# Optimization experiments

Hardware: AMD Instinct MI355X
Metric: run time of the kernel (lower is better)

The kernel has to match this reference:

```python
import jax, jax.numpy as jnp
import numpy as np

D_MODEL = 1024
NHEAD = 16
NUM_KV = 4
D_K = D_MODEL // NHEAD          # 64
GROUP = NHEAD // NUM_KV          # 4 query heads per kv head
ROPE_BASE = 10000.0


def _rope(x, seq_len):
    """Apply rotary embedding. x: [B, h, S, d_k], positions 0..seq_len-1."""
    half = D_K // 2
    inv_freq = 1.0 / (ROPE_BASE ** (jnp.arange(0, D_K, 2, dtype=jnp.float32) / D_K))
    t = jnp.arange(seq_len, dtype=jnp.float32)
    freqs = jnp.outer(t, inv_freq)                      # [S, d_k/2]
    emb = jnp.concatenate([freqs, freqs], axis=-1)      # [S, d_k]
    cos, sin = jnp.cos(emb), jnp.sin(emb)               # broadcast over B, h
    x1, x2 = x[..., :half], x[..., half:]
    rot = jnp.concatenate([-x2, x1], axis=-1)
    return x * cos + rot * sin


def setup_inputs() -> dict:
    key = jax.random.key(0)
    ks = jax.random.split(key, 12)
    B, S = 2, 2048
    s_in = 1.0 / np.sqrt(D_MODEL)
    inp = {
        "query": jax.random.normal(ks[0], (B, S, D_MODEL), jnp.float32),
        "key":   jax.random.normal(ks[1], (B, S, D_MODEL), jnp.float32),
        "value": jax.random.normal(ks[2], (B, S, D_MODEL), jnp.float32),
        "Wq": jax.random.normal(ks[3], (D_MODEL, D_MODEL), jnp.float32) * s_in,
        "bq": jnp.zeros((D_MODEL,), jnp.float32),
        "Wk": jax.random.normal(ks[4], (NUM_KV * D_K, D_MODEL), jnp.float32) * s_in,
        "bk": jnp.zeros((NUM_KV * D_K,), jnp.float32),
        "Wv": jax.random.normal(ks[5], (NUM_KV * D_K, D_MODEL), jnp.float32) * s_in,
        "bv": jnp.zeros((NUM_KV * D_K,), jnp.float32),
        "Wo": jax.random.normal(ks[6], (D_MODEL, D_MODEL), jnp.float32) * s_in,
        "bo": jnp.zeros((D_MODEL,), jnp.float32),
    }
    return inp


def reference(query, key, value, Wq, bq, Wk, bk, Wv, bv, Wo, bo):
    B, S, _ = query.shape
    T = key.shape[1]
    # projections (torch Linear: x @ W^T + b)
    Q = (query @ Wq.T + bq).reshape(B, S, NHEAD, D_K).transpose(0, 2, 1, 3)   # [B,H,S,dk]
    K = (key   @ Wk.T + bk).reshape(B, T, NUM_KV, D_K).transpose(0, 2, 1, 3)  # [B,KV,T,dk]
    V = (value @ Wv.T + bv).reshape(B, T, NUM_KV, D_K).transpose(0, 2, 1, 3)
    # fused RoPE (start_pos = 0)
    Q = _rope(Q, S)
    K = _rope(K, T)
    # expand kv heads (repeat_interleave on head dim)
    Kr = jnp.repeat(K, GROUP, axis=1)   # [B,H,T,dk]
    Vr = jnp.repeat(V, GROUP, axis=1)
    scale = 1.0 / np.sqrt(D_K)
    scores = jnp.einsum("bhsd,bhtd->bhst", Q, Kr) * scale   # [B,H,S,T]
    attn = jax.nn.softmax(scores, axis=-1)                    # dropout = eval/no-op
    context = jnp.einsum("bhst,bhtd->bhsd", attn, Vr)        # [B,H,S,dk]
    context = context.transpose(0, 2, 1, 3).reshape(B, S, D_MODEL)
    return context @ Wo.T + bo
```

## Files before the change

### kernel.cpp

```cpp
#include <hip/hip_runtime.h>
#include <hip/hip_bf16.h>

typedef __hip_bfloat16 bf16;
typedef __attribute__((ext_vector_type(8))) short short8;
typedef __attribute__((ext_vector_type(4))) short short4v;
typedef __attribute__((ext_vector_type(4))) float f32x4;
typedef __attribute__((ext_vector_type(4))) float float4v;

static __device__ inline short f2bf(float f){
  __hip_bfloat16 h = __float2bfloat16(f);
  return *reinterpret_cast<short*>(&h);
}

static __device__ __forceinline__ unsigned cvt_pk_bf16(float lo, float hi){
  unsigned r;
  asm("v_cvt_pk_bf16_f32 %0, %1, %2" : "=v"(r) : "v"(lo), "v"(hi));
  return r;
}

static __device__ __forceinline__ float exp2_fast(float x){
  float r;
  asm("v_exp_f32 %0, %1" : "=v"(r) : "v"(x));
  return r;
}

static __device__ inline short8 load8(const float* p){
  float4v a = *reinterpret_cast<const float4v*>(p);
  float4v b = *reinterpret_cast<const float4v*>(p + 4);
  short8 r;
  unsigned* u = reinterpret_cast<unsigned*>(&r);
  u[0] = cvt_pk_bf16(a[0], a[1]);
  u[1] = cvt_pk_bf16(a[2], a[3]);
  u[2] = cvt_pk_bf16(b[0], b[1]);
  u[3] = cvt_pk_bf16(b[2], b[3]);
  return r;
}
static __device__ inline short8 load8(const bf16* p){
  return *reinterpret_cast<const short8*>(p);
}

typedef __attribute__((address_space(1))) const unsigned int gas_u32;
typedef __attribute__((address_space(3))) unsigned int las_u32;
static __device__ __forceinline__ void gload16(const void* g, void* l){
  __builtin_amdgcn_global_load_lds((gas_u32*)g, (las_u32*)l, 16, 0, 0);
}

template<int N>
static __device__ __forceinline__ void vm_barrier(){
  if constexpr (N == 8) asm volatile("s_waitcnt vmcnt(8)" ::: "memory");
  else if constexpr (N == 4) asm volatile("s_waitcnt vmcnt(4)" ::: "memory");
  else if constexpr (N == 2) asm volatile("s_waitcnt vmcnt(2)" ::: "memory");
  else asm volatile("s_waitcnt vmcnt(0)" ::: "memory");
  __builtin_amdgcn_s_barrier();
  __builtin_amdgcn_sched_barrier(0);
}

#define CVT_Q   0
#define CVT_K   4194304
#define CVT_V   8388608
#define CVT_WQ  12582912
#define CVT_WK  13631488
#define CVT_WV  13893632
#define CVT_WO  14155776
#define CVT_TOT 15204352
__global__ void cvt_kernel(bf16* __restrict__ dst, float* __restrict__ tab,
    const float* q, const float* k, const float* v,
    const float* wq, const float* wk, const float* wv, const float* wo){
  if (blockIdx.x < 256){
    const int idx = blockIdx.x * 256 + threadIdx.x;
    const int d = idx & 31, s = idx >> 5;
    const float ang = (float)s * exp2f(-0.41524101186092030f * (float)d);
    float sn, cs;
    sincosf(ang, &sn, &cs);
    tab[idx*2] = cs; tab[idx*2+1] = sn;
  }
  const size_t i8 = ((size_t)blockIdx.x * 256 + threadIdx.x) * 8;
  const float* src; size_t off;
  if      (i8 < CVT_K ){ src = q;  off = i8; }
  else if (i8 < CVT_V ){ src = k;  off = i8 - CVT_K; }
  else if (i8 < CVT_WQ){ src = v;  off = i8 - CVT_V; }
  else if (i8 < CVT_WK){ src = wq; off = i8 - CVT_WQ; }
  else if (i8 < CVT_WV){ src = wk; off = i8 - CVT_WK; }
  else if (i8 < CVT_WO){ src = wv; off = i8 - CVT_WV; }
  else                 { src = wo; off = i8 - CVT_WO; }
  *reinterpret_cast<short8*>(reinterpret_cast<short*>(dst) + i8) = load8(src + off);
}

template<int MODE>
__device__ __forceinline__ void gemm_bt_v2(
    short* lds, void* __restrict__ Cout,
    const bf16* __restrict__ A, const bf16* __restrict__ B,
    const float* __restrict__ bias, const float* __restrict__ tab,
    int ntile, int mtile, int N, int K)
{
  const int NK = K >> 5;
  const int n0 = ntile * 128, m0 = mtile * 128;
  const int tid = threadIdx.x, w = tid >> 6, lane = tid & 63;
  const int wm = w >> 1, wn = w & 1, lr = lane & 15, lg = lane >> 4;
  const int r0 = w*32 + (lane >> 2), r1 = r0 + 16;
  const int c0 = ((lane & 3) ^ ((r0 >> 1) & 3)) * 8;
  const int c1 = ((lane & 3) ^ ((r1 >> 1) & 3)) * 8;
  const bf16* A0 = A + (size_t)(m0 + r0) * K + c0;
  const bf16* A1 = A + (size_t)(m0 + r1) * K + c1;
  const bf16* B0 = B + (size_t)(n0 + r0) * K + c0;
  const bf16* B1 = B + (size_t)(n0 + r1) * K + c1;
  const int ldsW = (w*32) * 32;
  int offA[4], offB[4];
  #pragma unroll
  for (int i = 0; i < 4; i++){
    const int ra = wm*64 + i*16 + lr;
    offA[i] = ra*64 + ((lg ^ ((ra >> 1) & 3)) * 16);
    const int rb = wn*64 + i*16 + lr;
    offB[i] = rb*64 + ((lg ^ ((rb >> 1) & 3)) * 16);
  }
  auto stage = [&](int t){
    short* bufA = lds + (t & 3) * 8192;
    short* bufB = bufA + 4096;
    gload16(A0 + t*32, bufA + ldsW);
    gload16(A1 + t*32, bufA + ldsW + 512);
    gload16(B0 + t*32, bufB + ldsW);
    gload16(B1 + t*32, bufB + ldsW + 512);
  };
  f32x4 acc[4][4] = {};
  stage(0); stage(1);
  for (int t = 0; t < NK; t++){
    if (t + 2 < NK){ stage(t + 2); vm_barrier<8>(); }
    else if (t + 1 < NK){ vm_barrier<4>(); }
    else { vm_barrier<0>(); }
    const char* bufA = (const char*)(lds + (t & 3) * 8192);
    const char* bufB = bufA + 8192;
    short8 af[4], bfm[4];
    #pragma unroll
    for (int mt = 0; mt < 4; mt++) af[mt]  = *(const short8*)(bufA + offA[mt]);
    #pragma unroll
    for (int nt = 0; nt < 4; nt++) bfm[nt] = *(const short8*)(bufB + offB[nt]);
    __builtin_amdgcn_s_setprio(1);
    #pragma unroll
    for (int mt = 0; mt < 4; mt++)
      #pragma unroll
      for (int nt = 0; nt < 4; nt++)
        acc[mt][nt] = __builtin_amdgcn_mfma_f32_16x16x32_bf16(af[mt], bfm[nt], acc[mt][nt], 0, 0, 0);
    __builtin_amdgcn_s_setprio(0);
  }
  if constexpr (MODE == 0){
    float* C = (float*)Cout;
    #pragma unroll
    for (int mt = 0; mt < 4; mt++){
      #pragma unroll
      for (int nt = 0; nt < 4; nt++){
        const int col = n0 + wn*64 + nt*16 + lr;
        const float bv = bias[col];
        const int rbase = m0 + wm*64 + mt*16 + lg*4;
        #pragma unroll
        for (int i = 0; i < 4; i++)
          C[(size_t)(rbase + i) * N + col] = acc[mt][nt][i] + bv;
      }
    }
  } else if constexpr (MODE == 1 || MODE == 2){
    bf16* dst = (bf16*)Cout;
    constexpr int NH = (MODE == 1) ? 16 : 4;
    constexpr float SC = (MODE == 1) ? 0.18033688011112042f : 1.0f;
    #pragma unroll
    for (int mt = 0; mt < 4; mt++){
      #pragma unroll
      for (int nt = 0; nt < 2; nt++){
        const int col = n0 + wn*64 + nt*16 + lr;
        const int d = col & 63;
        const int hh = col >> 6;
        const float b1 = bias[col], b2 = bias[col + 32];
        #pragma unroll
        for (int i = 0; i < 4; i++){
          const int m = m0 + wm*64 + mt*16 + lg*4 + i;
          const int s = m & 2047, bb = m >> 11;
          const float cs = tab[(s*32 + d)*2], sn = tab[(s*32 + d)*2 + 1];
          const float x1 = acc[mt][nt][i] + b1;
          const float x2 = acc[mt][nt+2][i] + b2;
          const size_t o = ((size_t)(bb*NH + hh) * 2048 + s) * 64 + d;
          dst[o]      = __float2bfloat16((x1*cs - x2*sn) * SC);
          dst[o + 32] = __float2bfloat16((x2*cs + x1*sn) * SC);
        }
      }
    }
  } else {
    bf16* dst = (bf16*)Cout;
    #pragma unroll
    for (int mt = 0; mt < 4; mt++){
      #pragma unroll
      for (int nt = 0; nt < 4; nt++){
        const int col = n0 + wn*64 + nt*16 + lr;
        const int kv = col >> 6, d = col & 63;
        const float bv = bias[col];
        #pragma unroll
        for (int i = 0; i < 4; i++){
          const int m = m0 + wm*64 + mt*16 + lg*4 + i;
          const int s = m & 2047, bb = m >> 11;
          dst[((size_t)(bb*4 + kv) * 64 + d) * 2048 + s] = __float2bfloat16(acc[mt][nt][i] + bv);
        }
      }
    }
  }
}

__global__ __launch_bounds__(256, 2) void gemm_qkv_kernel(
    bf16* Qa, bf16* Ka, bf16* Va, const bf16* cvt,
    const float* bq, const float* bk, const float* bv, const float* tab){
  __shared__ short lds[4 * 8192];
  const int pid = blockIdx.x;
  const int x = pid >> 5;
  const int y = (pid & 7) * 4 + ((pid >> 3) & 3);
  if (x < 8)
    gemm_bt_v2<1>(lds, Qa, cvt + CVT_Q, cvt + CVT_WQ, bq, tab, x,    y, 1024, 1024);
  else if (x < 10)
    gemm_bt_v2<2>(lds, Ka, cvt + CVT_K, cvt + CVT_WK, bk, tab, x-8,  y, 256, 1024);
  else
    gemm_bt_v2<3>(lds, Va, cvt + CVT_V, cvt + CVT_WV, bv, tab, x-10, y, 256, 1024);
}
__global__ __launch_bounds__(256, 2) void gemm_out_kernel(
    float* C, const bf16* ctx, const bf16* cvt, const float* bo){
  __shared__ short lds[4 * 8192];
  const int pid = blockIdx.x;
  const int x = pid >> 5;
  const int y = (pid & 7) * 4 + ((pid >> 3) & 3);
  gemm_bt_v2<0>(lds, C, ctx, cvt + CVT_WO, bo, nullptr, x, y, 1024, 1024);
}

__global__ __launch_bounds__(256, 2) void attn_kernel(
    bf16* __restrict__ ctx, const bf16* __restrict__ Qa,
    const bf16* __restrict__ Ka, const bf16* __restrict__ Vt)
{
  __shared__ short Klds[2][128 * 64];
  __shared__ short Vlds[2][64 * 128];
  const int pid = blockIdx.y * 16 + blockIdx.x;
  const int bh = (pid & 7) * 4 + ((pid >> 3) & 3);
  const int q0 = (pid >> 5) * 128;
  const int b = bh >> 4, h = bh & 15, kvh = h >> 2;
  const int tid = threadIdx.x, w = tid >> 6, lane = tid & 63;
  const int lr = lane & 15, lg = lane >> 4;
  const bf16* Qbase = Qa + (size_t)bh * 2048 * 64;
  const bf16* Kbase = Ka + (size_t)(b*4 + kvh) * 2048 * 64;
  const bf16* Vbase = Vt + (size_t)(b*4 + kvh) * 64 * 2048;

  short8 qf[2][2];
  #pragma unroll
  for (int qt = 0; qt < 2; qt++){
    qf[qt][0] = load8(Qbase + (size_t)(q0 + w*32 + qt*16 + lr) * 64 + lg*8);
    qf[qt][1] = load8(Qbase + (size_t)(q0 + w*32 + qt*16 + lr) * 64 + 32 + lg*8);
  }

  const int xswk = (lr & 7) << 4;
  const int koff0 = lr*128 + ((lg*16) ^ xswk);
  const int koff1 = lr*128 + ((64 + lg*16) ^ xswk);
  int voff[4][2];
  #pragma unroll
  for (int kkA = 0; kkA < 4; kkA++)
    #pragma unroll
    for (int hh = 0; hh < 2; hh++)
      voff[kkA][hh] = lr*256 + (((kkA*4 + hh*2 + (lg >> 1)) ^ lr) << 4) + (lg & 1)*8;

  const int l8 = lane >> 3;
  const int chk = (lane & 7) ^ l8;
  const bf16* kSrc = Kbase + (size_t)(w*32 + l8) * 64 + chk*8;
  const int vr0 = lane >> 4;
  const bf16* vSrc[4];
  #pragma unroll
  for (int j = 0; j < 4; j++)
    vSrc[j] = Vbase + (size_t)(w*16 + j*4 + vr0) * 2048 + ((lane & 15) ^ (j*4 + vr0)) * 8;

  auto stage = [&](int bi, int t){
    short* Kd = &Klds[bi][(w*32) * 64];
    short* Vd = &Vlds[bi][(w*16) * 128];
    const bf16* ks = kSrc + (size_t)t * 8192;
    #pragma unroll
    for (int j = 0; j < 4; j++) gload16(ks + j*512, Kd + j*512);
    #pragma unroll
    for (int j = 0; j < 4; j++) gload16(vSrc[j] + t*128, Vd + j*512);
  };

  f32x4 o[2][4] = {};
  f32x4 acc_l[2] = {};
  short8 ones;
  #pragma unroll
  for (int j = 0; j < 4; j++) reinterpret_cast<unsigned*>(&ones)[j] = 0x3F803F80u;

  f32x4 st[8][2];

  stage(0, 0);
  vm_barrier<0>();

  for (int t = 0; t < 16; t++){
    if (t + 1 < 16) stage((t+1) & 1, t+1);

    const char* Kc = (const char*)&Klds[t & 1][0];
    __builtin_amdgcn_s_setprio(1);
    #pragma unroll
    for (int mt = 0; mt < 8; mt++){
      short8 kf0 = *reinterpret_cast<const short8*>(Kc + mt*2048 + koff0);
      short8 kf1 = *reinterpret_cast<const short8*>(Kc + mt*2048 + koff1);
      #pragma unroll
      for (int qt = 0; qt < 2; qt++){
        st[mt][qt] = __builtin_amdgcn_mfma_f32_16x16x32_bf16(kf0, qf[qt][0], (f32x4){0.f,0.f,0.f,0.f}, 0, 0, 0);
        st[mt][qt] = __builtin_amdgcn_mfma_f32_16x16x32_bf16(kf1, qf[qt][1], st[mt][qt], 0, 0, 0);
      }
    }
    __builtin_amdgcn_s_setprio(0);

    short8 pf[2][4];
    #pragma unroll
    for (int qt = 0; qt < 2; qt++){
      unsigned* pw = reinterpret_cast<unsigned*>(&pf[qt][0]);
      #pragma unroll
      for (int p = 0; p < 16; p++){
        const int mt = p >> 1, i0 = (p & 1) * 2;
        const float e0 = exp2_fast(st[mt][qt][i0]);
        const float e1 = exp2_fast(st[mt][qt][i0 + 1]);
        pw[p] = cvt_pk_bf16(e0, e1);
      }
    }

    const char* Vc = (const char*)&Vlds[t & 1][0];
    __builtin_amdgcn_s_setprio(1);
    #pragma unroll
    for (int qt = 0; qt < 2; qt++)
      #pragma unroll
      for (int kkA = 0; kkA < 4; kkA++)
        acc_l[qt] = __builtin_amdgcn_mfma_f32_16x16x32_bf16(pf[qt][kkA], ones, acc_l[qt], 0, 0, 0);
    #pragma unroll
    for (int dt = 0; dt < 4; dt++){
      #pragma unroll
      for (int kkA = 0; kkA < 4; kkA++){
        short8 vf;
        *reinterpret_cast<short4v*>(&vf) =
            *reinterpret_cast<const short4v*>(Vc + dt*4096 + voff[kkA][0]);
        *reinterpret_cast<short4v*>(reinterpret_cast<short*>(&vf) + 4) =
            *reinterpret_cast<const short4v*>(Vc + dt*4096 + voff[kkA][1]);
        #pragma unroll
        for (int qt = 0; qt < 2; qt++)
          o[qt][dt] = __builtin_amdgcn_mfma_f32_16x16x32_bf16(pf[qt][kkA], vf, o[qt][dt], 0, 0, 0);
      }
    }
    __builtin_amdgcn_s_setprio(0);

    if (t + 1 < 16) vm_barrier<0>();
  }

  #pragma unroll
  for (int qt = 0; qt < 2; qt++){
    float lb[4];
    #pragma unroll
    for (int i = 0; i < 4; i++) lb[i] = 1.0f / acc_l[qt][i];
    #pragma unroll
    for (int dt = 0; dt < 4; dt++){
      #pragma unroll
      for (int i = 0; i < 4; i++){
        const int q = q0 + w*32 + qt*16 + lg*4 + i;
        ctx[(size_t)(b*2048 + q) * 1024 + h*64 + dt*16 + lr] =
            __float2bfloat16(o[qt][dt][i] * lb[i]);
      }
    }
  }
}

extern "C" void kernel_launch(void* const* d_in, const int* in_sizes, int n_in,
                              void* d_out, int out_size, void* d_ws, size_t ws_size,
                              hipStream_t stream)
{
  const float* query = (const float*)d_in[0];
  const float* key   = (const float*)d_in[1];
  const float* value = (const float*)d_in[2];
  const float* Wq = (const float*)d_in[3];
  const float* bq = (const float*)d_in[4];
  const float* Wk = (const float*)d_in[5];
  const float* bk = (const float*)d_in[6];
  const float* Wv = (const float*)d_in[7];
  const float* bv = (const float*)d_in[8];
  const float* Wo = (const float*)d_in[9];
  const float* bo = (const float*)d_in[10];
  float* out = (float*)d_out;

  char* ws = (char*)d_ws;
  size_t off = 0;
  float* tab = (float*)(ws + off); off += (size_t)2048 * 32 * 2 * 4;
  bf16*  Qa  = (bf16*)(ws + off);  off += (size_t)32 * 2048 * 64 * 2;
  bf16*  Ka  = (bf16*)(ws + off);  off += (size_t)8 * 2048 * 64 * 2;
  bf16*  Va  = (bf16*)(ws + off);  off += (size_t)8 * 64 * 2048 * 2;
  bf16*  ctx = (bf16*)(ws + off);  off += (size_t)2 * 2048 * 1024 * 2;
  bf16*  cvt = (bf16*)(ws + off);  off += (size_t)CVT_TOT * 2;

  cvt_kernel<<<CVT_TOT / 8 / 256, 256, 0, stream>>>(cvt, tab, query, key, value, Wq, Wk, Wv, Wo);
  gemm_qkv_kernel<<<384, 256, 0, stream>>>(Qa, Ka, Va, cvt, bq, bk, bv, tab);
  attn_kernel<<<dim3(16, 32), 256, 0, stream>>>(ctx, Qa, Ka, Va);
  gemm_out_kernel<<<256, 256, 0, stream>>>(out, ctx, cvt, bo);
}
```

Before: 96.67 us.

## Switch attention kernel MFMAs from 16x16x32 to 32x32x16 bf16 tiles

```diff
diff --git a/kernel.cpp b/kernel.cpp
--- a/kernel.cpp
+++ b/kernel.cpp
@@ -5,6 +5,7 @@
 typedef __attribute__((ext_vector_type(8))) short short8;
 typedef __attribute__((ext_vector_type(4))) short short4v;
 typedef __attribute__((ext_vector_type(4))) float f32x4;
+typedef __attribute__((ext_vector_type(16))) float f32x16;
 typedef __attribute__((ext_vector_type(4))) float float4v;
 
 static __device__ inline short f2bf(float f){
@@ -235,27 +236,24 @@
   const int q0 = (pid >> 5) * 128;
   const int b = bh >> 4, h = bh & 15, kvh = h >> 2;
   const int tid = threadIdx.x, w = tid >> 6, lane = tid & 63;
-  const int lr = lane & 15, lg = lane >> 4;
+  const int l31 = lane & 31, l5 = lane >> 5;
   const bf16* Qbase = Qa + (size_t)bh * 2048 * 64;
   const bf16* Kbase = Ka + (size_t)(b*4 + kvh) * 2048 * 64;
   const bf16* Vbase = Vt + (size_t)(b*4 + kvh) * 64 * 2048;
 
-  short8 qf[2][2];
-  #pragma unroll
-  for (int qt = 0; qt < 2; qt++){
-    qf[qt][0] = load8(Qbase + (size_t)(q0 + w*32 + qt*16 + lr) * 64 + lg*8);
-    qf[qt][1] = load8(Qbase + (size_t)(q0 + w*32 + qt*16 + lr) * 64 + 32 + lg*8);
-  }
-
-  const int xswk = (lr & 7) << 4;
-  const int koff0 = lr*128 + ((lg*16) ^ xswk);
-  const int koff1 = lr*128 + ((64 + lg*16) ^ xswk);
-  int voff[4][2];
-  #pragma unroll
-  for (int kkA = 0; kkA < 4; kkA++)
-    #pragma unroll
-    for (int hh = 0; hh < 2; hh++)
-      voff[kkA][hh] = lr*256 + (((kkA*4 + hh*2 + (lg >> 1)) ^ lr) << 4) + (lg & 1)*8;
+  short8 qf32[4];
+  #pragma unroll
+  for (int ks = 0; ks < 4; ks++)
+    qf32[ks] = load8(Qbase + (size_t)(q0 + w*32 + l31) * 64 + ks*16 + l5*8);
+
+  int koff32[4];
+  #pragma unroll
+  for (int ks = 0; ks < 4; ks++)
+    koff32[ks] = l31*128 + (((ks*2 + l5) ^ (lane & 7)) << 4);
+  int voff32[16];
+  #pragma unroll
+  for (int g = 0; g < 16; g++)
+    voff32[g] = l31*256 + ((g ^ (lane & 15)) << 4) + l5*8;
 
   const int l8 = lane >> 3;
   const int chk = (lane & 7) ^ l8;
@@ -276,13 +274,11 @@
     for (int j = 0; j < 4; j++) gload16(vSrc[j] + t*128, Vd + j*512);
   };
 
-  f32x4 o[2][4] = {};
-  f32x4 acc_l[2] = {};
+  f32x16 o32[2] = {};
+  f32x16 acc_l = {};
   short8 ones;
   #pragma unroll
   for (int j = 0; j < 4; j++) reinterpret_cast<unsigned*>(&ones)[j] = 0x3F803F80u;
-
-  f32x4 st[8][2];
 
   stage(0, 0);
   vm_barrier<0>();
@@ -291,71 +287,72 @@
     if (t + 1 < 16) stage((t+1) & 1, t+1);
 
     const char* Kc = (const char*)&Klds[t & 1][0];
+    f32x16 st32[4];
     __builtin_amdgcn_s_setprio(1);
     #pragma unroll
-    for (int mt = 0; mt < 8; mt++){
-      short8 kf0 = *reinterpret_cast<const short8*>(Kc + mt*2048 + koff0);
-      short8 kf1 = *reinterpret_cast<const short8*>(Kc + mt*2048 + koff1);
-      #pragma unroll
-      for (int qt = 0; qt < 2; qt++){
-        st[mt][qt] = __builtin_amdgcn_mfma_f32_16x16x32_bf16(kf0, qf[qt][0], (f32x4){0.f,0.f,0.f,0.f}, 0, 0, 0);
-        st[mt][qt] = __builtin_amdgcn_mfma_f32_16x16x32_bf16(kf1, qf[qt][1], st[mt][qt], 0, 0, 0);
-      }
+    for (int kvblk = 0; kvblk < 4; kvblk++){
+      f32x16 acc = {};
+      #pragma unroll
+      for (int ks = 0; ks < 4; ks++){
+        short8 kf = *reinterpret_cast<const short8*>(Kc + kvblk*4096 + koff32[ks]);
+        acc = __builtin_amdgcn_mfma_f32_32x32x16_bf16(kf, qf32[ks], acc, 0, 0, 0);
+      }
+      st32[kvblk] = acc;
     }
     __builtin_amdgcn_s_setprio(0);
 
-    short8 pf[2][4];
-    #pragma unroll
-    for (int qt = 0; qt < 2; qt++){
-      unsigned* pw = reinterpret_cast<unsigned*>(&pf[qt][0]);
-      #pragma unroll
-      for (int p = 0; p < 16; p++){
-        const int mt = p >> 1, i0 = (p & 1) * 2;
-        const float e0 = exp2_fast(st[mt][qt][i0]);
-        const float e1 = exp2_fast(st[mt][qt][i0 + 1]);
-        pw[p] = cvt_pk_bf16(e0, e1);
-      }
-    }
-
     const char* Vc = (const char*)&Vlds[t & 1][0];
-    __builtin_amdgcn_s_setprio(1);
-    #pragma unroll
-    for (int qt = 0; qt < 2; qt++)
-      #pragma unroll
-      for (int kkA = 0; kkA < 4; kkA++)
-        acc_l[qt] = __builtin_amdgcn_mfma_f32_16x16x32_bf16(pf[qt][kkA], ones, acc_l[qt], 0, 0, 0);
-    #pragma unroll
-    for (int dt = 0; dt < 4; dt++){
-      #pragma unroll
-      for (int kkA = 0; kkA < 4; kkA++){
-        short8 vf;
-        *reinterpret_cast<short4v*>(&vf) =
-            *reinterpret_cast<const short4v*>(Vc + dt*4096 + voff[kkA][0]);
-        *reinterpret_cast<short4v*>(reinterpret_cast<short*>(&vf) + 4) =
-            *reinterpret_cast<const short4v*>(Vc + dt*4096 + voff[kkA][1]);
-        #pragma unroll
-        for (int qt = 0; qt < 2; qt++)
-          o[qt][dt] = __builtin_amdgcn_mfma_f32_16x16x32_bf16(pf[qt][kkA], vf, o[qt][dt], 0, 0, 0);
-      }
-    }
-    __builtin_amdgcn_s_setprio(0);
+    #pragma unroll
+    for (int kvblk = 0; kvblk < 4; kvblk++){
+      float e[16];
+      #pragma unroll
+      for (int r = 0; r < 16; r++) e[r] = exp2_fast(st32[kvblk][r]);
+      short8 pa0, pa1;
+      unsigned* p0 = reinterpret_cast<unsigned*>(&pa0);
+      unsigned* p1 = reinterpret_cast<unsigned*>(&pa1);
+      #pragma unroll
+      for (int j2 = 0; j2 < 4; j2++){
+        p0[j2] = cvt_pk_bf16(e[2*j2],     e[2*j2 + 1]);
+        p1[j2] = cvt_pk_bf16(e[8 + 2*j2], e[8 + 2*j2 + 1]);
+      }
+      __builtin_amdgcn_s_setprio(1);
+      acc_l = __builtin_amdgcn_mfma_f32_32x32x16_bf16(pa0, ones, acc_l, 0, 0, 0);
+      acc_l = __builtin_amdgcn_mfma_f32_32x32x16_bf16(pa1, ones, acc_l, 0, 0, 0);
+      #pragma unroll
+      for (int dblk = 0; dblk < 2; dblk++){
+        {
+          short8 vf;
+          *reinterpret_cast<short4v*>(&vf) =
+              *reinterpret_cast<const short4v*>(Vc + dblk*8192 + voff32[kvblk*4 + 0]);
+          *reinterpret_cast<short4v*>(reinterpret_cast<short*>(&vf) + 4) =
+              *reinterpret_cast<const short4v*>(Vc + dblk*8192 + voff32[kvblk*4 + 1]);
+          o32[dblk] = __builtin_amdgcn_mfma_f32_32x32x16_bf16(pa0, vf, o32[dblk], 0, 0, 0);
+        }
+        {
+          short8 vf;
+          *reinterpret_cast<short4v*>(&vf) =
+              *reinterpret_cast<const short4v*>(Vc + dblk*8192 + voff32[kvblk*4 + 2]);
+          *reinterpret_cast<short4v*>(reinterpret_cast<short*>(&vf) + 4) =
+              *reinterpret_cast<const short4v*>(Vc + dblk*8192 + voff32[kvblk*4 + 3]);
+          o32[dblk] = __builtin_amdgcn_mfma_f32_32x32x16_bf16(pa1, vf, o32[dblk], 0, 0, 0);
+        }
+      }
+      __builtin_amdgcn_s_setprio(0);
+    }
 
     if (t + 1 < 16) vm_barrier<0>();
   }
 
-  #pragma unroll
-  for (int qt = 0; qt < 2; qt++){
-    float lb[4];
-    #pragma unroll
-    for (int i = 0; i < 4; i++) lb[i] = 1.0f / acc_l[qt][i];
-    #pragma unroll
-    for (int dt = 0; dt < 4; dt++){
-      #pragma unroll
-      for (int i = 0; i < 4; i++){
-        const int q = q0 + w*32 + qt*16 + lg*4 + i;
-        ctx[(size_t)(b*2048 + q) * 1024 + h*64 + dt*16 + lr] =
-            __float2bfloat16(o[qt][dt][i] * lb[i]);
-      }
+  float lb[16];
+  #pragma unroll
+  for (int r = 0; r < 16; r++) lb[r] = 1.0f / acc_l[r];
+  #pragma unroll
+  for (int dblk = 0; dblk < 2; dblk++){
+    #pragma unroll
+    for (int r = 0; r < 16; r++){
+      const int q = q0 + w*32 + (r & 3) + 8*(r >> 2) + 4*l5;
+      ctx[(size_t)(b*2048 + q) * 1024 + h*64 + dblk*32 + l31] =
+          __float2bfloat16(o32[dblk][r] * lb[r]);
     }
   }
 }
```

New measurement: 100.8 us. 4.3% more time.
